# Optimization experiments

Measured on AMD Instinct MI355X. Metric: run time of the kernel, lower is better.

Reference implementation:

```python
import jax, jax.numpy as jnp
import numpy as np

NUM_CLASSES = 33  # labels 0..32; class 0 = background, 32 instances
EPS = 1e-06


def _lovasz_hinge_flat(logits, labels):
    # logits, labels: flat 1-D float arrays (labels in {0,1})
    signs = 2.0 * labels - 1.0
    errors = 1.0 - logits * signs
    order = jnp.argsort(-errors)            # descending sort
    errors_sorted = errors[order]
    gt_sorted = labels[order]
    gts = jnp.sum(gt_sorted)
    intersection = gts - jnp.cumsum(gt_sorted)
    union = gts + jnp.cumsum(1.0 - gt_sorted)
    jaccard = 1.0 - intersection / union
    grad = jnp.concatenate([jaccard[:1], jaccard[1:] - jaccard[:-1]])
    return jnp.dot(jax.nn.relu(errors_sorted), grad)


def _per_sample_loss(y_emb, y_sig, gt_patch):
    # y_emb: [2,H,W] float, y_sig: [1,H,W] float, gt_patch: [1,H,W] int
    # to_onehot(gt)[0, 1:] -> [N,H,W], N = NUM_CLASSES-1 instance channels
    gt_one_hot = jax.nn.one_hot(gt_patch[0], NUM_CLASSES, axis=0, dtype=y_emb.dtype)[1:]
    counts = jnp.sum(gt_one_hot, axis=(1, 2), keepdims=True)          # [N,1,1]
    # per-instance embedding centers: [2,N,1,1]
    centers = jnp.sum(gt_one_hot[None] * y_emb[:, None], axis=(2, 3), keepdims=True) / counts
    instance_sigmas = gt_one_hot[None] * y_sig[:, None]               # [1,N,H,W]
    sigmas = jnp.sum(instance_sigmas, axis=(2, 3), keepdims=True) / counts  # [1,N,1,1]
    var_sigmas = jnp.sum(((instance_sigmas - jax.lax.stop_gradient(sigmas)) * gt_one_hot) ** 2) / counts  # [N,1,1]
    center_dist = jnp.linalg.norm(centers - y_emb[:, None], axis=0)   # [N,H,W]
    probs = jnp.exp(-0.5 * (center_dist / sigmas) ** 2)               # [1,N,H,W]
    logits = (probs * 2.0 - 1.0).reshape(-1)
    labels = jnp.broadcast_to(gt_one_hot[None], probs.shape).reshape(-1)
    return _lovasz_hinge_flat(logits, labels) + jnp.mean(var_sigmas)


def setup_inputs() -> dict:
    key = jax.random.key(0)
    k1, k2, k3 = jax.random.split(key, 3)
    B, H, W = 4, 512, 512
    y_embeddings = jax.random.normal(k1, (B, 2, H, W), dtype=jnp.float32)
    y_sigma = jax.random.uniform(k2, (B, 1, H, W), dtype=jnp.float32)
    y_true = jax.random.randint(k3, (B, 1, H, W), 0, NUM_CLASSES, dtype=jnp.int64)
    return {"y_embeddings": y_embeddings, "y_sigma": y_sigma, "y_true": y_true}


def reference(y_embeddings, y_sigma, y_true):
    # Assumes every sample contains foreground (random labels over 512x512
    # guarantee this w.h.p.), so the torch `if torch.any(gt>0)` branch is taken
    # for all samples and the final loss is the mean over the batch.
    losses = jax.vmap(_per_sample_loss)(y_embeddings, y_sigma, y_true)
    return jnp.mean(losses)
```

## Files before the change

kernel.cpp:

```cpp
#include <hip/hip_runtime.h>

#define HW    262144
#define BNUM  4
#define NC    33
#define NI    32

#define NB     2048
#define TMAX   16.0f
#define BSCALE 128.0f
#define EG     8192
#define ESCALE 4096.0f

#define W_TH   0
#define W_E0   4096
#define W_E1   (W_E0 + NC)
#define W_SS   (W_E1 + NC)
#define W_CNT  (W_SS + NC)
#define W_SVAR (W_CNT + NC)
#define W_SIG  (W_SVAR + 1)
#define W_Q    (W_SIG + NC)
#define W_C0   (W_Q + NC)
#define W_C1   (W_C0 + NC)
#define W_LOSS (W_C1 + NC)
#define W_STRIDE 4368

__global__ void __launch_bounds__(256) stats_kernel(
    const float* __restrict__ emb, const float* __restrict__ sig,
    const int* __restrict__ gt, float* __restrict__ ws) {
  int s = blockIdx.y;
  float* wsS = ws + (size_t)s * W_STRIDE;
  __shared__ float a0[4][NC], a1[4][NC], as_[4][NC];
  __shared__ unsigned ac[4][NC];
  int t = threadIdx.x;
  int w = t >> 6;
  for (int k = t; k < 4 * NC; k += 256) {
    ((float*)a0)[k] = 0.f; ((float*)a1)[k] = 0.f; ((float*)as_)[k] = 0.f;
    ((unsigned*)ac)[k] = 0u;
  }
  __syncthreads();
  const float* e0p = emb + (size_t)s * 2 * HW;
  const float* e1p = e0p + HW;
  const float* sp  = sig + (size_t)s * HW;
  const int*   gp  = gt  + (size_t)s * HW;
  int base = blockIdx.x * 1024;
  #pragma unroll
  for (int i = 0; i < 2; ++i) {
    int idx = base + i * 512 + t * 2;
    int2  lb = *(const int2*)(gp + idx);
    float2 x = *(const float2*)(e0p + idx);
    float2 y = *(const float2*)(e1p + idx);
    float2 sg = *(const float2*)(sp + idx);
    if (lb.x > 0) {
      atomicAdd(&a0[w][lb.x], x.x); atomicAdd(&a1[w][lb.x], y.x);
      atomicAdd(&as_[w][lb.x], sg.x); atomicAdd(&ac[w][lb.x], 1u);
    }
    if (lb.y > 0) {
      atomicAdd(&a0[w][lb.y], x.y); atomicAdd(&a1[w][lb.y], y.y);
      atomicAdd(&as_[w][lb.y], sg.y); atomicAdd(&ac[w][lb.y], 1u);
    }
  }
  __syncthreads();
  if (t >= 1 && t < NC) {
    float s0 = a0[0][t] + a0[1][t] + a0[2][t] + a0[3][t];
    float s1 = a1[0][t] + a1[1][t] + a1[2][t] + a1[3][t];
    float ss = as_[0][t] + as_[1][t] + as_[2][t] + as_[3][t];
    unsigned c = ac[0][t] + ac[1][t] + ac[2][t] + ac[3][t];
    if (c) {
      atomicAdd(&wsS[W_E0 + t], s0);
      atomicAdd(&wsS[W_E1 + t], s1);
      atomicAdd(&wsS[W_SS + t], ss);
      atomicAdd((unsigned*)wsS + (W_CNT + t), c);
    }
  }
}

__global__ void prep_kernel(float* __restrict__ ws) {
  int s = blockIdx.x;
  float* wsS = ws + (size_t)s * W_STRIDE;
  const unsigned* wsu = (const unsigned*)wsS;
  int n = threadIdx.x;
  if (n >= 1 && n < NC) {
    float inv = 1.0f / (float)wsu[W_CNT + n];
    float sg = wsS[W_SS + n] * inv;
    wsS[W_SIG + n] = sg;
    wsS[W_Q + n]   = 0.5f / (sg * sg);
    wsS[W_C0 + n]  = wsS[W_E0 + n] * inv;
    wsS[W_C1 + n]  = wsS[W_E1 + n] * inv;
  }
}

__global__ void __launch_bounds__(512) hist_kernel(
    const float* __restrict__ emb, const float* __restrict__ sig,
    const int* __restrict__ gt, float* __restrict__ ws) {
  int s = blockIdx.y;
  float* wsS = ws + (size_t)s * W_STRIDE;
  __shared__ unsigned hist[NB * 4];
  __shared__ float c0s[NC], c1s[NC], qs[NC], sgs[NC];
  __shared__ float vred[8];
  int t = threadIdx.x;
  int r = t & 3;
  for (int k = t; k < NB * 4; k += 512) hist[k] = 0u;
  if (t < NC) {
    c0s[t] = wsS[W_C0 + t]; c1s[t] = wsS[W_C1 + t];
    qs[t]  = wsS[W_Q + t];  sgs[t] = wsS[W_SIG + t];
  }
  __syncthreads();
  const float* e0p = emb + (size_t)s * 2 * HW;
  const float* e1p = e0p + HW;
  const float* sp  = sig + (size_t)s * HW;
  const int*   gp  = gt  + (size_t)s * HW;
  int idx = blockIdx.x * 1024 + t * 2;
  int2   lb = *(const int2*)(gp + idx);
  float2 px = *(const float2*)(e0p + idx);
  float2 py = *(const float2*)(e1p + idx);
  float2 sg = *(const float2*)(sp + idx);
  float vs = 0.f;
  if (lb.x > 0) { float d = sg.x - sgs[lb.x]; vs += d * d; }
  if (lb.y > 0) { float d = sg.y - sgs[lb.y]; vs += d * d; }
  #pragma unroll 4
  for (int n = 1; n <= NI; ++n) {
    float c0 = c0s[n], c1 = c1s[n], q = qs[n];
    {
      float dx = c0 - px.x, dy = c1 - py.x;
      float tt = (dx * dx + dy * dy) * q;
      bool pos = (lb.x == n);
      if (pos || tt < TMAX) {
        int b = (int)(tt * BSCALE); if (b > NB - 1) b = NB - 1;
        atomicAdd(&hist[(b << 2) | r], pos ? 0x10000u : 1u);
      }
    }
    {
      float dx = c0 - px.y, dy = c1 - py.y;
      float tt = (dx * dx + dy * dy) * q;
      bool pos = (lb.y == n);
      if (pos || tt < TMAX) {
        int b = (int)(tt * BSCALE); if (b > NB - 1) b = NB - 1;
        atomicAdd(&hist[(b << 2) | r], pos ? 0x10000u : 1u);
      }
    }
  }
  for (int o = 32; o; o >>= 1) vs += __shfl_down(vs, o);
  if ((t & 63) == 0) vred[t >> 6] = vs;
  __syncthreads();
  if (t == 0) {
    float tot = 0.f;
    for (int i = 0; i < 8; ++i) tot += vred[i];
    atomicAdd(&wsS[W_SVAR], tot);
  }
  unsigned long long* th = (unsigned long long*)wsS;
  for (int k = t; k < NB; k += 512) {
    unsigned v = hist[k * 4] + hist[k * 4 + 1] + hist[k * 4 + 2] + hist[k * 4 + 3];
    if (v) {
      unsigned long long add = ((unsigned long long)(v >> 16) << 32) | (v & 0xFFFFu);
      atomicAdd(&th[k], add);
    }
  }
}

__global__ void __launch_bounds__(512) scan_kernel(float* __restrict__ ws) {
  int s = blockIdx.x;
  float* wsS = ws + (size_t)s * W_STRIDE;
  const unsigned long long* th = (const unsigned long long*)wsS;
  const unsigned* wsu = (const unsigned*)wsS;
  __shared__ unsigned ep[EG], en[EG];
  __shared__ unsigned snp[512], snn[512];
  __shared__ unsigned tot[2];
  __shared__ float red[512];
  int t = threadIdx.x;
  for (int k = t; k < EG; k += 512) { ep[k] = 0u; en[k] = 0u; }
  __syncthreads();
  for (int b = t; b < NB; b += 512) {
    unsigned long long v = th[b];
    unsigned pos = (unsigned)(v >> 32), neg = (unsigned)(v & 0xFFFFFFFFu);
    if (pos | neg) {
      float tc = ((float)b + 0.5f) * (1.0f / BSCALE);
      float ex = __expf(-tc);
      if (pos) {
        float e = 2.0f - 2.0f * ex;
        int k = (int)(e * ESCALE); if (k > EG - 1) k = EG - 1;
        atomicAdd(&ep[k], pos);
      }
      if (neg) {
        float e = 2.0f * ex;
        int k = (int)(e * ESCALE); if (k > EG - 1) k = EG - 1;
        atomicAdd(&en[k], neg);
      }
    }
  }
  __syncthreads();
  const int CH = EG / 512;
  int j0 = t * CH;
  unsigned np = 0, nn = 0;
  for (int k = 0; k < CH; ++k) {
    int b = EG - 1 - (j0 + k);
    np += ep[b]; nn += en[b];
  }
  snp[t] = np; snn[t] = nn;
  __syncthreads();
  if (t == 0) {
    unsigned ap = 0, an = 0;
    for (int i = 0; i < 512; ++i) {
      unsigned x = snp[i]; snp[i] = ap; ap += x;
      x = snn[i]; snn[i] = an; an += x;
    }
    tot[0] = ap; tot[1] = an;
  }
  __syncthreads();
  float P = (float)tot[0];
  unsigned p = snp[t], f = snn[t];
  float jprev = 1.0f - (P - (float)p) / (P + (float)f);
  float contrib = 0.f;
  for (int k = 0; k < CH; ++k) {
    int b = EG - 1 - (j0 + k);
    unsigned ap_ = ep[b], an_ = en[b];
    if (ap_ | an_) {
      p += ap_; f += an_;
      float j = 1.0f - (P - (float)p) / (P + (float)f);
      float e = ((float)b + 0.5f) * (2.0f / EG);
      contrib += e * (j - jprev);
      jprev = j;
    }
  }
  red[t] = contrib;
  __syncthreads();
  for (int o = 256; o; o >>= 1) {
    if (t < o) red[t] += red[t + o];
    __syncthreads();
  }
  if (t == 0) {
    float vsum = 0.f;
    for (int n = 1; n < NC; ++n) vsum += 1.0f / (float)wsu[W_CNT + n];
    wsS[W_LOSS] = red[0] + wsS[W_SVAR] * vsum / (float)NI;
  }
}

__global__ void final_kernel(const float* __restrict__ ws, float* __restrict__ out) {
  float a = 0.f;
  for (int s = 0; s < BNUM; ++s) a += ws[(size_t)s * W_STRIDE + W_LOSS];
  out[0] = 0.25f * a;
}

extern "C" void kernel_launch(void* const* d_in, const int* in_sizes, int n_in,
                              void* d_out, int out_size, void* d_ws, size_t ws_size,
                              hipStream_t stream) {
  const float* emb = (const float*)d_in[0];
  const float* sig = (const float*)d_in[1];
  const int*   gt  = (const int*)d_in[2];
  float* out = (float*)d_out;
  float* ws  = (float*)d_ws;

  hipMemsetAsync(d_ws, 0, (size_t)BNUM * W_STRIDE * sizeof(float), stream);

  dim3 gA(256, BNUM);
  stats_kernel<<<gA, 256, 0, stream>>>(emb, sig, gt, ws);
  prep_kernel<<<BNUM, 64, 0, stream>>>(ws);
  dim3 gB(256, BNUM);
  hist_kernel<<<gB, 512, 0, stream>>>(emb, sig, gt, ws);
  scan_kernel<<<BNUM, 512, 0, stream>>>(ws);
  final_kernel<<<1, 1, 0, stream>>>(ws, out);
}
```

Baseline: 141.0 us.

## Compute sigma variance via sum of squares, drop prep kernel, warp-level scans

The stats kernel now also accumulates the sum of squared sigmas per instance, so the variance term becomes S2 - c*mean^2 and no second pass over sigma is needed. The hist kernel stops reading the sigma array and computes the centers and q inline, which removes the separate prep kernel launch. The scan kernel replaces its serial single-thread prefix and its tree reduction with wave shuffle scans. The one-pass variance formula risks float cancellation.

```diff
diff --git a/kernel.cpp b/kernel.cpp
--- a/kernel.cpp
+++ b/kernel.cpp
@@ -11,30 +11,29 @@
 #define EG     8192
 #define ESCALE 4096.0f
 
+typedef unsigned long long ull;
+
 #define W_TH   0
 #define W_E0   4096
 #define W_E1   (W_E0 + NC)
 #define W_SS   (W_E1 + NC)
-#define W_CNT  (W_SS + NC)
-#define W_SVAR (W_CNT + NC)
-#define W_SIG  (W_SVAR + 1)
-#define W_Q    (W_SIG + NC)
-#define W_C0   (W_Q + NC)
-#define W_C1   (W_C0 + NC)
-#define W_LOSS (W_C1 + NC)
-#define W_STRIDE 4368
+#define W_SS2  (W_SS + NC)
+#define W_CNT  (W_SS2 + NC)
+#define W_LOSS (W_CNT + NC)
+#define W_STRIDE 4272
 
 __global__ void __launch_bounds__(256) stats_kernel(
     const float* __restrict__ emb, const float* __restrict__ sig,
     const int* __restrict__ gt, float* __restrict__ ws) {
   int s = blockIdx.y;
   float* wsS = ws + (size_t)s * W_STRIDE;
-  __shared__ float a0[4][NC], a1[4][NC], as_[4][NC];
+  __shared__ float a0[4][NC], a1[4][NC], as_[4][NC], as2[4][NC];
   __shared__ unsigned ac[4][NC];
   int t = threadIdx.x;
   int w = t >> 6;
   for (int k = t; k < 4 * NC; k += 256) {
-    ((float*)a0)[k] = 0.f; ((float*)a1)[k] = 0.f; ((float*)as_)[k] = 0.f;
+    ((float*)a0)[k] = 0.f; ((float*)a1)[k] = 0.f;
+    ((float*)as_)[k] = 0.f; ((float*)as2)[k] = 0.f;
     ((unsigned*)ac)[k] = 0u;
   }
   __syncthreads();
@@ -52,11 +51,13 @@
     float2 sg = *(const float2*)(sp + idx);
     if (lb.x > 0) {
       atomicAdd(&a0[w][lb.x], x.x); atomicAdd(&a1[w][lb.x], y.x);
-      atomicAdd(&as_[w][lb.x], sg.x); atomicAdd(&ac[w][lb.x], 1u);
+      atomicAdd(&as_[w][lb.x], sg.x); atomicAdd(&as2[w][lb.x], sg.x * sg.x);
+      atomicAdd(&ac[w][lb.x], 1u);
     }
     if (lb.y > 0) {
       atomicAdd(&a0[w][lb.y], x.y); atomicAdd(&a1[w][lb.y], y.y);
-      atomicAdd(&as_[w][lb.y], sg.y); atomicAdd(&ac[w][lb.y], 1u);
+      atomicAdd(&as_[w][lb.y], sg.y); atomicAdd(&as2[w][lb.y], sg.y * sg.y);
+      atomicAdd(&ac[w][lb.y], 1u);
     }
   }
   __syncthreads();
@@ -64,59 +65,43 @@
     float s0 = a0[0][t] + a0[1][t] + a0[2][t] + a0[3][t];
     float s1 = a1[0][t] + a1[1][t] + a1[2][t] + a1[3][t];
     float ss = as_[0][t] + as_[1][t] + as_[2][t] + as_[3][t];
+    float s2 = as2[0][t] + as2[1][t] + as2[2][t] + as2[3][t];
     unsigned c = ac[0][t] + ac[1][t] + ac[2][t] + ac[3][t];
     if (c) {
       atomicAdd(&wsS[W_E0 + t], s0);
       atomicAdd(&wsS[W_E1 + t], s1);
       atomicAdd(&wsS[W_SS + t], ss);
+      atomicAdd(&wsS[W_SS2 + t], s2);
       atomicAdd((unsigned*)wsS + (W_CNT + t), c);
     }
   }
 }
 
-__global__ void prep_kernel(float* __restrict__ ws) {
-  int s = blockIdx.x;
-  float* wsS = ws + (size_t)s * W_STRIDE;
-  const unsigned* wsu = (const unsigned*)wsS;
-  int n = threadIdx.x;
-  if (n >= 1 && n < NC) {
-    float inv = 1.0f / (float)wsu[W_CNT + n];
-    float sg = wsS[W_SS + n] * inv;
-    wsS[W_SIG + n] = sg;
-    wsS[W_Q + n]   = 0.5f / (sg * sg);
-    wsS[W_C0 + n]  = wsS[W_E0 + n] * inv;
-    wsS[W_C1 + n]  = wsS[W_E1 + n] * inv;
-  }
-}
-
 __global__ void __launch_bounds__(512) hist_kernel(
-    const float* __restrict__ emb, const float* __restrict__ sig,
-    const int* __restrict__ gt, float* __restrict__ ws) {
+    const float* __restrict__ emb, const int* __restrict__ gt,
+    float* __restrict__ ws) {
   int s = blockIdx.y;
   float* wsS = ws + (size_t)s * W_STRIDE;
   __shared__ unsigned hist[NB * 4];
-  __shared__ float c0s[NC], c1s[NC], qs[NC], sgs[NC];
-  __shared__ float vred[8];
+  __shared__ float c0s[NC], c1s[NC], qs[NC];
   int t = threadIdx.x;
   int r = t & 3;
   for (int k = t; k < NB * 4; k += 512) hist[k] = 0u;
-  if (t < NC) {
-    c0s[t] = wsS[W_C0 + t]; c1s[t] = wsS[W_C1 + t];
-    qs[t]  = wsS[W_Q + t];  sgs[t] = wsS[W_SIG + t];
+  if (t >= 1 && t < NC) {
+    float inv = 1.0f / (float)((const unsigned*)wsS)[W_CNT + t];
+    c0s[t] = wsS[W_E0 + t] * inv;
+    c1s[t] = wsS[W_E1 + t] * inv;
+    float sg = wsS[W_SS + t] * inv;
+    qs[t] = 0.5f / (sg * sg);
   }
   __syncthreads();
   const float* e0p = emb + (size_t)s * 2 * HW;
   const float* e1p = e0p + HW;
-  const float* sp  = sig + (size_t)s * HW;
   const int*   gp  = gt  + (size_t)s * HW;
   int idx = blockIdx.x * 1024 + t * 2;
   int2   lb = *(const int2*)(gp + idx);
   float2 px = *(const float2*)(e0p + idx);
   float2 py = *(const float2*)(e1p + idx);
-  float2 sg = *(const float2*)(sp + idx);
-  float vs = 0.f;
-  if (lb.x > 0) { float d = sg.x - sgs[lb.x]; vs += d * d; }
-  if (lb.y > 0) { float d = sg.y - sgs[lb.y]; vs += d * d; }
   #pragma unroll 4
   for (int n = 1; n <= NI; ++n) {
     float c0 = c0s[n], c1 = c1s[n], q = qs[n];
@@ -139,19 +124,12 @@
       }
     }
   }
-  for (int o = 32; o; o >>= 1) vs += __shfl_down(vs, o);
-  if ((t & 63) == 0) vred[t >> 6] = vs;
-  __syncthreads();
-  if (t == 0) {
-    float tot = 0.f;
-    for (int i = 0; i < 8; ++i) tot += vred[i];
-    atomicAdd(&wsS[W_SVAR], tot);
-  }
-  unsigned long long* th = (unsigned long long*)wsS;
+  __syncthreads();
+  ull* th = (ull*)wsS;
   for (int k = t; k < NB; k += 512) {
     unsigned v = hist[k * 4] + hist[k * 4 + 1] + hist[k * 4 + 2] + hist[k * 4 + 3];
     if (v) {
-      unsigned long long add = ((unsigned long long)(v >> 16) << 32) | (v & 0xFFFFu);
+      ull add = ((ull)(v >> 16) << 32) | (v & 0xFFFFu);
       atomicAdd(&th[k], add);
     }
   }
@@ -160,17 +138,32 @@
 __global__ void __launch_bounds__(512) scan_kernel(float* __restrict__ ws) {
   int s = blockIdx.x;
   float* wsS = ws + (size_t)s * W_STRIDE;
-  const unsigned long long* th = (const unsigned long long*)wsS;
+  const ull* th = (const ull*)wsS;
   const unsigned* wsu = (const unsigned*)wsS;
   __shared__ unsigned ep[EG], en[EG];
-  __shared__ unsigned snp[512], snn[512];
-  __shared__ unsigned tot[2];
-  __shared__ float red[512];
+  __shared__ ull wsum[8];
+  __shared__ float red[8];
+  __shared__ float vart_s;
   int t = threadIdx.x;
+  int lane = t & 63, wid = t >> 6;
   for (int k = t; k < EG; k += 512) { ep[k] = 0u; en[k] = 0u; }
+  if (wid == 0) {
+    float S = 0.f, rc = 0.f;
+    if (lane >= 1 && lane < NC) {
+      float c = (float)wsu[W_CNT + lane];
+      float sg = wsS[W_SS + lane] / c;
+      S = wsS[W_SS2 + lane] - c * sg * sg;
+      rc = 1.0f / c;
+    }
+    for (int o = 32; o; o >>= 1) {
+      S  += __shfl_down(S, o);
+      rc += __shfl_down(rc, o);
+    }
+    if (lane == 0) vart_s = S * rc / (float)NI;
+  }
   __syncthreads();
   for (int b = t; b < NB; b += 512) {
-    unsigned long long v = th[b];
+    ull v = th[b];
     unsigned pos = (unsigned)(v >> 32), neg = (unsigned)(v & 0xFFFFFFFFu);
     if (pos | neg) {
       float tc = ((float)b + 0.5f) * (1.0f / BSCALE);
@@ -195,19 +188,23 @@
     int b = EG - 1 - (j0 + k);
     np += ep[b]; nn += en[b];
   }
-  snp[t] = np; snn[t] = nn;
-  __syncthreads();
-  if (t == 0) {
-    unsigned ap = 0, an = 0;
-    for (int i = 0; i < 512; ++i) {
-      unsigned x = snp[i]; snp[i] = ap; ap += x;
-      x = snn[i]; snn[i] = an; an += x;
-    }
-    tot[0] = ap; tot[1] = an;
-  }
-  __syncthreads();
-  float P = (float)tot[0];
-  unsigned p = snp[t], f = snn[t];
+  ull v = ((ull)np << 32) | (ull)nn;
+  ull inc = v;
+  for (int o = 1; o < 64; o <<= 1) {
+    ull u = __shfl_up(inc, o);
+    if (lane >= o) inc += u;
+  }
+  if (lane == 63) wsum[wid] = inc;
+  __syncthreads();
+  ull offset = 0, total = 0;
+  for (int i = 0; i < 8; ++i) {
+    ull x = wsum[i];
+    if (i < wid) offset += x;
+    total += x;
+  }
+  ull excl = offset + inc - v;
+  float P = (float)(unsigned)(total >> 32);
+  unsigned p = (unsigned)(excl >> 32), f = (unsigned)(excl & 0xFFFFFFFFu);
   float jprev = 1.0f - (P - (float)p) / (P + (float)f);
   float contrib = 0.f;
   for (int k = 0; k < CH; ++k) {
@@ -221,16 +218,13 @@
       jprev = j;
     }
   }
-  red[t] = contrib;
-  __syncthreads();
-  for (int o = 256; o; o >>= 1) {
-    if (t < o) red[t] += red[t + o];
-    __syncthreads();
-  }
+  for (int o = 32; o; o >>= 1) contrib += __shfl_down(contrib, o);
+  if (lane == 0) red[wid] = contrib;
+  __syncthreads();
   if (t == 0) {
-    float vsum = 0.f;
-    for (int n = 1; n < NC; ++n) vsum += 1.0f / (float)wsu[W_CNT + n];
-    wsS[W_LOSS] = red[0] + wsS[W_SVAR] * vsum / (float)NI;
+    float tot = 0.f;
+    for (int i = 0; i < 8; ++i) tot += red[i];
+    wsS[W_LOSS] = tot + vart_s;
   }
 }
 
@@ -253,9 +247,8 @@
 
   dim3 gA(256, BNUM);
   stats_kernel<<<gA, 256, 0, stream>>>(emb, sig, gt, ws);
-  prep_kernel<<<BNUM, 64, 0, stream>>>(ws);
   dim3 gB(256, BNUM);
-  hist_kernel<<<gB, 512, 0, stream>>>(emb, sig, gt, ws);
+  hist_kernel<<<gB, 512, 0, stream>>>(emb, gt, ws);
   scan_kernel<<<BNUM, 512, 0, stream>>>(ws);
   final_kernel<<<1, 1, 0, stream>>>(ws, out);
 }
```

Result: faster. 133.9 us (-5.0%).
